# Optimization experiments

Measured on AMD Instinct MI355X. Metric: run time of the kernel, lower is better.

The kernel has to match this reference:

```python
import jax, jax.numpy as jnp
import numpy as np

B, C, N, M, H = 2, 512, 2048, 2048, 8
HD = C // H
SCALE = HD ** -0.5


def setup_inputs() -> dict:
    key = jax.random.key(0)
    ks = jax.random.split(key, 8)
    x = jax.random.normal(ks[0], (B, C, N), dtype=jnp.float32)
    y = jax.random.normal(ks[1], (B, C, M), dtype=jnp.float32)
    # linear weights stored as [in, out] so out = in @ W (equivalent to torch Linear)
    Wq = jax.random.normal(ks[2], (C, C), dtype=jnp.float32) * (C ** -0.5)
    Wkv = jax.random.normal(ks[3], (C, 2 * C), dtype=jnp.float32) * (C ** -0.5)
    # depthwise Conv1d, kernel_size=1, groups=C -> per-channel scale + bias
    lw = jax.random.normal(ks[4], (C,), dtype=jnp.float32)
    lb = jax.random.normal(ks[5], (C,), dtype=jnp.float32) * 0.01
    Wp = jax.random.normal(ks[6], (C, C), dtype=jnp.float32) * (C ** -0.5)
    bp = jax.random.normal(ks[7], (C,), dtype=jnp.float32) * 0.01
    return {"x": x, "y": y, "Wq": Wq, "Wkv": Wkv, "lw": lw, "lb": lb, "Wp": Wp, "bp": bp}


def reference(x, y, Wq, Wkv, lw, lb, Wp, bp):
    # x: [B,C,N], y: [B,C,M]
    q = (x.transpose(0, 2, 1) @ Wq).reshape(B, N, H, HD).transpose(0, 2, 1, 3)  # [B,H,N,HD]
    kv = (y.transpose(0, 2, 1) @ Wkv).reshape(B, M, H, HD, 2).transpose(0, 2, 1, 3, 4)
    k, v = kv[..., 0], kv[..., 1]  # [B,H,M,HD]
    attn = jax.nn.softmax(jnp.einsum('bhnd,bhmd->bhnm', q, k) * SCALE, axis=-1)
    # depthwise conv1d (ksize=1) on v laid out as [B,C,M]; channel c = h*HD + d
    lw2 = lw.reshape(H, HD)[None, :, None, :]
    lb2 = lb.reshape(H, HD)[None, :, None, :]
    v = v + v * lw2 + lb2
    out = jnp.einsum('bhnm,bhmd->bhnd', attn, v).transpose(0, 2, 1, 3).reshape(B, N, C)
    out = (out @ Wp + bp).transpose(0, 2, 1)  # [B,C,N]
    return out
```

## Files before the change

### kernel.cpp

```cpp
#include <hip/hip_runtime.h>

#define Bb 2
#define Cc 512
#define Nn 2048
#define Mm 2048
#define Hh 8
#define HD 64
#define QSCALE 0.18033688011112042f

typedef unsigned short u16;
typedef unsigned int u32;
typedef __bf16 bf16x8 __attribute__((ext_vector_type(8)));
typedef float f32x16 __attribute__((ext_vector_type(16)));

union V4 {
    uint4 u;
    bf16x8 b;
};

__device__ __forceinline__ u16 f2bfu(float f) {
    unsigned int b = __float_as_uint(f);
    unsigned int r = (b + 0x7fffu + ((b >> 16) & 1u)) >> 16;
    return (u16)r;
}
__device__ __forceinline__ float bfu2f(u16 u) {
    return __uint_as_float(((unsigned int)u) << 16);
}
__device__ __forceinline__ u32 pkbf(float lo, float hi_) {
    return __builtin_amdgcn_perm(__float_as_uint(hi_) + 0x8000u,
                                 __float_as_uint(lo) + 0x8000u, 0x07060302u);
}

__global__ __launch_bounds__(256) void transpose_xy(const float* __restrict__ x,
                                                    const float* __restrict__ y,
                                                    u16* __restrict__ xT,
                                                    u16* __restrict__ yT) {
    __shared__ float tile[32][33];
    const int z = blockIdx.z;
    const float* in = (z < 2) ? x : y;
    u16* out = (z < 2) ? xT : yT;
    const int b = z & 1;
    const int R = 512, S = 2048;
    size_t base = (size_t)b * R * S;
    int r0 = blockIdx.y * 32, s0 = blockIdx.x * 32;
    int tx = threadIdx.x, ty = threadIdx.y;
#pragma unroll
    for (int k = 0; k < 4; k++)
        tile[ty + 8 * k][tx] = in[base + (size_t)(r0 + ty + 8 * k) * S + s0 + tx];
    __syncthreads();
#pragma unroll
    for (int k = 0; k < 4; k++)
        out[base + (size_t)(s0 + ty + 8 * k) * R + r0 + tx] = f2bfu(tile[tx][ty + 8 * k]);
}

__global__ __launch_bounds__(256) void transpose_w(const float* __restrict__ Wq,
                                                   const float* __restrict__ Wkv,
                                                   const float* __restrict__ Wp,
                                                   u16* __restrict__ WqT,
                                                   u16* __restrict__ WkvT,
                                                   u16* __restrict__ WpT) {
    __shared__ float tile[32][33];
    const int bx = blockIdx.x;
    const float* in;
    u16* out;
    int S, sx;
    if (bx < 16) {
        in = Wq; out = WqT; S = 512; sx = bx;
    } else if (bx < 48) {
        in = Wkv; out = WkvT; S = 1024; sx = bx - 16;
    } else {
        in = Wp; out = WpT; S = 512; sx = bx - 48;
    }
    const int R = 512;
    int r0 = blockIdx.y * 32, s0 = sx * 32;
    int tx = threadIdx.x, ty = threadIdx.y;
#pragma unroll
    for (int k = 0; k < 4; k++)
        tile[ty + 8 * k][tx] = in[(size_t)(r0 + ty + 8 * k) * S + s0 + tx];
    __syncthreads();
#pragma unroll
    for (int k = 0; k < 4; k++)
        out[(size_t)(s0 + ty + 8 * k) * R + r0 + tx] = f2bfu(tile[tx][ty + 8 * k]);
}

template <int MODE>
__global__ __launch_bounds__(256) void gemm_nt(const u16* __restrict__ A,
                                               const u16* __restrict__ Bt,
                                               u16* __restrict__ outp, int Ncols) {
    __shared__ alignas(16) u16 As[2][128 * 64];
    __shared__ alignas(16) u16 Bs[2][64 * 64];
    const int t = threadIdx.x;
    const int lane = t & 63, w = t >> 6;
    const int r = lane & 31, hi = lane >> 5;
    const int r0 = blockIdx.y * 128, c0 = blockIdx.x * 64;
    const int wr = (w & 1) * 64, wc = (w >> 1) * 32;

    const int sra = t >> 3, ska = t & 7;
    const int swa = ((ska ^ (sra & 7)) << 3);
    const u16* Ag = A + (size_t)(r0 + sra) * 512 + ska * 8;
    const u16* Bg = Bt + (size_t)(c0 + sra) * 512 + ska * 8;

    {
#pragma unroll
        for (int i = 0; i < 4; i++)
            *(uint4*)&As[0][(sra + 32 * i) * 64 + swa] = *(const uint4*)(Ag + (size_t)i * 32 * 512);
#pragma unroll
        for (int i = 0; i < 2; i++)
            *(uint4*)&Bs[0][(sra + 32 * i) * 64 + swa] = *(const uint4*)(Bg + (size_t)i * 32 * 512);
    }
    __syncthreads();

    f32x16 acc[2];
#pragma unroll
    for (int rs = 0; rs < 2; rs++)
#pragma unroll
        for (int e = 0; e < 16; e++) acc[rs][e] = 0.f;

    const int ra0 = wr + r, ra1 = wr + 32 + r, rb = wc + r;

    for (int kk = 0; kk < 8; kk++) {
        const int cur = kk & 1;
        uint4 pa[4], pb[2];
        const bool more = (kk < 7);
        if (more) {
            const size_t ko = (size_t)(kk + 1) * 64;
#pragma unroll
            for (int i = 0; i < 4; i++) pa[i] = *(const uint4*)(Ag + (size_t)i * 32 * 512 + ko);
#pragma unroll
            for (int i = 0; i < 2; i++) pb[i] = *(const uint4*)(Bg + (size_t)i * 32 * 512 + ko);
        }
        V4 af[2][4], bf[4];
#pragma unroll
        for (int ks = 0; ks < 4; ks++) {
            const int c = 2 * ks + hi;
            bf[ks].u = *(const uint4*)&Bs[cur][rb * 64 + ((c ^ (rb & 7)) << 3)];
            af[0][ks].u = *(const uint4*)&As[cur][ra0 * 64 + ((c ^ (ra0 & 7)) << 3)];
            af[1][ks].u = *(const uint4*)&As[cur][ra1 * 64 + ((c ^ (ra1 & 7)) << 3)];
        }
#pragma unroll
        for (int ks = 0; ks < 4; ks++) {
            acc[0] = __builtin_amdgcn_mfma_f32_32x32x16_bf16(af[0][ks].b, bf[ks].b, acc[0], 0, 0, 0);
            acc[1] = __builtin_amdgcn_mfma_f32_32x32x16_bf16(af[1][ks].b, bf[ks].b, acc[1], 0, 0, 0);
        }
        if (more) {
            const int nxt = cur ^ 1;
#pragma unroll
            for (int i = 0; i < 4; i++) *(uint4*)&As[nxt][(sra + 32 * i) * 64 + swa] = pa[i];
#pragma unroll
            for (int i = 0; i < 2; i++) *(uint4*)&Bs[nxt][(sra + 32 * i) * 64 + swa] = pb[i];
        }
        __syncthreads();
    }

    const int cg = c0 + wc + r;
#pragma unroll
    for (int rs = 0; rs < 2; rs++)
#pragma unroll
        for (int e = 0; e < 16; e++) {
            int m = r0 + wr + rs * 32 + 4 * hi + (e & 3) + 8 * (e >> 2);
            float v = acc[rs][e];
            if constexpr (MODE == 3) v *= QSCALE;
            outp[(size_t)m * Ncols + cg] = f2bfu(v);
        }
}

__global__ __launch_bounds__(256) void gemm_out(const u16* __restrict__ Wt,
                                                const u16* __restrict__ Ob,
                                                float* __restrict__ out,
                                                const float* __restrict__ bias) {
    __shared__ alignas(16) u16 Ws[2][64 * 64];
    __shared__ alignas(16) u16 Os[2][128 * 64];
    const int t = threadIdx.x;
    const int lane = t & 63, w = t >> 6;
    const int r = lane & 31, hi = lane >> 5;
    const int c0 = blockIdx.x * 64, n0 = blockIdx.y * 128;
    const int cb = (w & 1) * 32, nb = (w >> 1) * 32;

    const int sra = t >> 3, ska = t & 7;
    const int swa = ((ska ^ (sra & 7)) << 3);
    const u16* Wg = Wt + (size_t)(c0 + sra) * 512 + ska * 8;
    const u16* Og = Ob + (size_t)(n0 + sra) * 512 + ska * 8;

    {
#pragma unroll
        for (int i = 0; i < 2; i++)
            *(uint4*)&Ws[0][(sra + 32 * i) * 64 + swa] = *(const uint4*)(Wg + (size_t)i * 32 * 512);
#pragma unroll
        for (int i = 0; i < 4; i++)
            *(uint4*)&Os[0][(sra + 32 * i) * 64 + swa] = *(const uint4*)(Og + (size_t)i * 32 * 512);
    }
    __syncthreads();

    f32x16 acc[2];
#pragma unroll
    for (int ns = 0; ns < 2; ns++)
#pragma unroll
        for (int e = 0; e < 16; e++) acc[ns][e] = 0.f;

    const int rw = cb + r, ro0 = nb + r, ro1 = nb + 64 + r;

    for (int kk = 0; kk < 8; kk++) {
        const int cur = kk & 1;
        uint4 pw[2], po_[4];
        const bool more = (kk < 7);
        if (more) {
            const size_t ko = (size_t)(kk + 1) * 64;
#pragma unroll
            for (int i = 0; i < 2; i++) pw[i] = *(const uint4*)(Wg + (size_t)i * 32 * 512 + ko);
#pragma unroll
            for (int i = 0; i < 4; i++) po_[i] = *(const uint4*)(Og + (size_t)i * 32 * 512 + ko);
        }
        V4 wf[4], of[2][4];
#pragma unroll
        for (int ks = 0; ks < 4; ks++) {
            const int c = 2 * ks + hi;
            wf[ks].u = *(const uint4*)&Ws[cur][rw * 64 + ((c ^ (rw & 7)) << 3)];
            of[0][ks].u = *(const uint4*)&Os[cur][ro0 * 64 + ((c ^ (ro0 & 7)) << 3)];
            of[1][ks].u = *(const uint4*)&Os[cur][ro1 * 64 + ((c ^ (ro1 & 7)) << 3)];
        }
#pragma unroll
        for (int ks = 0; ks < 4; ks++) {
            acc[0] = __builtin_amdgcn_mfma_f32_32x32x16_bf16(wf[ks].b, of[0][ks].b, acc[0], 0, 0, 0);
            acc[1] = __builtin_amdgcn_mfma_f32_32x32x16_bf16(wf[ks].b, of[1][ks].b, acc[1], 0, 0, 0);
        }
        if (more) {
            const int nxt = cur ^ 1;
#pragma unroll
            for (int i = 0; i < 2; i++) *(uint4*)&Ws[nxt][(sra + 32 * i) * 64 + swa] = pw[i];
#pragma unroll
            for (int i = 0; i < 4; i++) *(uint4*)&Os[nxt][(sra + 32 * i) * 64 + swa] = po_[i];
        }
        __syncthreads();
    }

#pragma unroll
    for (int e = 0; e < 16; e++) {
        const int c_r = c0 + cb + 4 * hi + (e & 3) + 8 * (e >> 2);
        const float bv = bias[c_r];
#pragma unroll
        for (int ns = 0; ns < 2; ns++) {
            const int rg = n0 + nb + ns * 64 + r;
            const int b = rg >> 11, n = rg & 2047;
            out[((size_t)b * 512 + c_r) * 2048 + n] = acc[ns][e] + bv;
        }
    }
}

__global__ __launch_bounds__(256) void split_kv(const u16* __restrict__ kv,
                                                const float* __restrict__ lw,
                                                const float* __restrict__ lb,
                                                u16* __restrict__ kout,
                                                u16* __restrict__ vtout) {
    __shared__ u16 vtile[64][72];
    int t = threadIdx.x;
    int m0 = blockIdx.x * 64, h = blockIdx.y, b = blockIdx.z;
    int mr = t >> 2, d0 = (t & 3) * 16;
    const u16* row = kv + ((size_t)(b * Mm + m0 + mr)) * 1024 + (h * 64 + d0) * 2;
    size_t kob = ((size_t)((b * Hh + h) * Mm) + m0 + mr) * 64 + d0;
#pragma unroll
    for (int i = 0; i < 16; i++) {
        int c = h * 64 + d0 + i;
        u16 kb = row[2 * i];
        float vv = bfu2f(row[2 * i + 1]);
        float vp = vv + vv * lw[c] + lb[c];
        kout[kob + i] = kb;
        vtile[d0 + i][mr] = f2bfu(vp);
    }
    __syncthreads();
    int dd = t >> 2, mg = (t & 3) * 16;
    size_t vob = ((size_t)((b * Hh + h) * 64) + dd) * Mm + m0 + mg;
#pragma unroll
    for (int i = 0; i < 16; i++) vtout[vob + i] = vtile[dd][mg + i];
}

__global__ __launch_bounds__(256, 4) void flash_attn(const u16* __restrict__ q,
                                                     const u16* __restrict__ kk,
                                                     const u16* __restrict__ vt,
                                                     float* __restrict__ po,
                                                     float* __restrict__ ls) {
    __shared__ alignas(16) u16 Ks[2][64 * 64];
    __shared__ alignas(16) u16 Vs[2][64 * 64];
    const int t = threadIdx.x;
    const int lane = t & 63, w = t >> 6;
    const int r = lane & 31, hi = lane >> 5;
    const int nt = blockIdx.x & 15, sp = blockIdx.x >> 4;
    const int h = blockIdx.y, b = blockIdx.z;
    const int bh = b * Hh + h;
    const int nw = nt * 128 + 32 * w + r;
    const int MT0 = sp * 8, MT1 = MT0 + 8;

    V4 qf[4];
    {
        const u16* qrow = q + ((size_t)(b * Nn + nw)) * Cc + h * HD + hi * 8;
#pragma unroll
        for (int ks = 0; ks < 4; ks++) qf[ks].u = *(const uint4*)(qrow + ks * 16);
    }

    const u16* kbase = kk + ((size_t)bh) * Mm * HD;
    const u16* vbase = vt + ((size_t)bh) * HD * Mm;

    const int cr0 = t >> 3, cc0 = t & 7;
    const int cr1 = cr0 + 32, cc1 = cc0;
    const int swa0 = cr0 * 64 + ((cc0 ^ (cr0 & 7)) << 3);
    const int swa1 = cr1 * 64 + ((cc1 ^ (cr1 & 7)) << 3);

    {
        int m00 = MT0 * 64;
        uint4 a0 = *(const uint4*)(kbase + (size_t)(m00 + cr0) * HD + cc0 * 8);
        uint4 a1 = *(const uint4*)(kbase + (size_t)(m00 + cr1) * HD + cc1 * 8);
        uint4 b0 = *(const uint4*)(vbase + (size_t)cr0 * Mm + m00 + cc0 * 8);
        uint4 b1 = *(const uint4*)(vbase + (size_t)cr1 * Mm + m00 + cc1 * 8);
        *(uint4*)&Ks[0][swa0] = a0;
        *(uint4*)&Ks[0][swa1] = a1;
        *(uint4*)&Vs[0][swa0] = b0;
        *(uint4*)&Vs[0][swa1] = b1;
    }
    __syncthreads();

    f32x16 oa0, oa1;
#pragma unroll
    for (int e = 0; e < 16; e++) {
        oa0[e] = 0.f;
        oa1[e] = 0.f;
    }
    float lsum = 0.f;

    for (int mt = MT0; mt < MT1; mt++) {
        const int cur = mt & 1;
        uint4 nk0, nk1, nv0, nv1;
        const bool more = (mt + 1 < MT1);
        if (more) {
            int m0 = (mt + 1) * 64;
            nk0 = *(const uint4*)(kbase + (size_t)(m0 + cr0) * HD + cc0 * 8);
            nk1 = *(const uint4*)(kbase + (size_t)(m0 + cr1) * HD + cc1 * 8);
            nv0 = *(const uint4*)(vbase + (size_t)cr0 * Mm + m0 + cc0 * 8);
            nv1 = *(const uint4*)(vbase + (size_t)cr1 * Mm + m0 + cc1 * 8);
        }
        f32x16 sa[2];
#pragma unroll
        for (int s = 0; s < 2; s++) {
#pragma unroll
            for (int e = 0; e < 16; e++) sa[s][e] = 0.f;
#pragma unroll
            for (int ks = 0; ks < 4; ks++) {
                V4 af;
                af.u = *(const uint4*)&Ks[cur][(32 * s + r) * 64 +
                                               (((2 * ks + hi) ^ (r & 7)) << 3)];
                sa[s] = __builtin_amdgcn_mfma_f32_32x32x16_bf16(af.b, qf[ks].b, sa[s], 0, 0, 0);
            }
        }
#pragma unroll
        for (int s = 0; s < 2; s++) {
            u32 p[8];
#pragma unroll
            for (int qq = 0; qq < 8; qq++) {
                float e0 = __builtin_amdgcn_exp2f(sa[s][2 * qq]);
                float e1 = __builtin_amdgcn_exp2f(sa[s][2 * qq + 1]);
                lsum += e0 + e1;
                p[qq] = pkbf(e0, e1);
            }
            u32 xr0 = __shfl_xor(hi ? p[0] : p[2], 32);
            u32 xr1 = __shfl_xor(hi ? p[1] : p[3], 32);
            u32 xr2 = __shfl_xor(hi ? p[4] : p[6], 32);
            u32 xr3 = __shfl_xor(hi ? p[5] : p[7], 32);
#pragma unroll
            for (int kl = 0; kl < 2; kl++) {
                V4 pf;
                if (kl == 0) {
                    pf.u.x = hi ? xr0 : p[0];
                    pf.u.y = hi ? xr1 : p[1];
                    pf.u.z = hi ? p[2] : xr0;
                    pf.u.w = hi ? p[3] : xr1;
                } else {
                    pf.u.x = hi ? xr2 : p[4];
                    pf.u.y = hi ? xr3 : p[5];
                    pf.u.z = hi ? p[6] : xr2;
                    pf.u.w = hi ? p[7] : xr3;
                }
                const int c = 4 * s + 2 * kl + hi;
                V4 vf0, vf1;
                vf0.u = *(const uint4*)&Vs[cur][r * 64 + ((c ^ (r & 7)) << 3)];
                vf1.u = *(const uint4*)&Vs[cur][(32 + r) * 64 + ((c ^ (r & 7)) << 3)];
                oa0 = __builtin_amdgcn_mfma_f32_32x32x16_bf16(vf0.b, pf.b, oa0, 0, 0, 0);
                oa1 = __builtin_amdgcn_mfma_f32_32x32x16_bf16(vf1.b, pf.b, oa1, 0, 0, 0);
            }
        }
        if (more) {
            const int nxt = cur ^ 1;
            *(uint4*)&Ks[nxt][swa0] = nk0;
            *(uint4*)&Ks[nxt][swa1] = nk1;
            *(uint4*)&Vs[nxt][swa0] = nv0;
            *(uint4*)&Vs[nxt][swa1] = nv1;
        }
        __syncthreads();
    }

    lsum += __shfl_xor(lsum, 32);
    float* pob = po + (((size_t)sp * 16 + bh) * 64) * 2048 + nw;
#pragma unroll
    for (int e = 0; e < 16; e++) {
        int d0 = (e & 3) + 8 * (e >> 2) + 4 * hi;
        pob[(size_t)d0 * 2048] = oa0[e];
        pob[(size_t)(d0 + 32) * 2048] = oa1[e];
    }
    if (hi == 0) ls[((size_t)sp * 16 + bh) * 2048 + nw] = lsum;
}

__global__ __launch_bounds__(256) void combine_o(const float* __restrict__ po,
                                                 const float* __restrict__ ls,
                                                 u16* __restrict__ o) {
    __shared__ u16 tile[64][72];
    const int t = threadIdx.x;
    const int n0 = blockIdx.x * 64, bh = blockIdx.y;
    const int n = n0 + (t & 63), dg = t >> 6;
    float linv;
    {
        float s = 0.f;
#pragma unroll
        for (int sp = 0; sp < 4; sp++) s += ls[((size_t)sp * 16 + bh) * 2048 + n];
        linv = 1.0f / s;
    }
#pragma unroll
    for (int i = 0; i < 16; i++) {
        int d = dg * 16 + i;
        float acc = 0.f;
#pragma unroll
        for (int sp = 0; sp < 4; sp++)
            acc += po[(((size_t)sp * 16 + bh) * 64 + d) * 2048 + n];
        tile[t & 63][d] = f2bfu(acc * linv);
    }
    __syncthreads();
    const int nr = t >> 2, dq = (t & 3) * 16;
    const int b = bh >> 3, h = bh & 7;
    u16* orow = o + ((size_t)(b * Nn + n0 + nr)) * Cc + h * 64 + dq;
    *(uint4*)(orow + 0) = *(const uint4*)&tile[nr][dq];
    *(uint4*)(orow + 8) = *(const uint4*)&tile[nr][dq + 8];
}

static const size_t OFF_XT = 0;
static const size_t OFF_YT = 4194304;
static const size_t OFF_WQT = 8388608;
static const size_t OFF_WKVT = 8912896;
static const size_t OFF_WPT = 9961472;
static const size_t OFF_Q = 10485760;
static const size_t OFF_KV = 14680064;
static const size_t OFF_K = 23068672;
static const size_t OFF_VT = 27262976;
static const size_t OFF_O = 31457280;
static const size_t OFF_PO = 35651584;
static const size_t OFF_LS = 69206016;

extern "C" void kernel_launch(void* const* d_in, const int* in_sizes, int n_in,
                              void* d_out, int out_size, void* d_ws, size_t ws_size,
                              hipStream_t stream) {
    const float* x = (const float*)d_in[0];
    const float* y = (const float*)d_in[1];
    const float* Wq = (const float*)d_in[2];
    const float* Wkv = (const float*)d_in[3];
    const float* lw = (const float*)d_in[4];
    const float* lb = (const float*)d_in[5];
    const float* Wp = (const float*)d_in[6];
    const float* bp = (const float*)d_in[7];

    char* ws = (char*)d_ws;
    u16* xT = (u16*)(ws + OFF_XT);
    u16* yT = (u16*)(ws + OFF_YT);
    u16* WqT = (u16*)(ws + OFF_WQT);
    u16* WkvT = (u16*)(ws + OFF_WKVT);
    u16* WpT = (u16*)(ws + OFF_WPT);
    u16* qb = (u16*)(ws + OFF_Q);
    u16* kvb = (u16*)(ws + OFF_KV);
    u16* kb = (u16*)(ws + OFF_K);
    u16* vtb = (u16*)(ws + OFF_VT);
    u16* ob = (u16*)(ws + OFF_O);
    float* po = (float*)(ws + OFF_PO);
    float* lsw = (float*)(ws + OFF_LS);

    dim3 tb(32, 8, 1);
    transpose_xy<<<dim3(64, 16, 4), tb, 0, stream>>>(x, y, xT, yT);
    transpose_w<<<dim3(64, 16), tb, 0, stream>>>(Wq, Wkv, Wp, WqT, WkvT, WpT);

    gemm_nt<3><<<dim3(8, 32), 256, 0, stream>>>(xT, WqT, qb, 512);
    gemm_nt<0><<<dim3(16, 32), 256, 0, stream>>>(yT, WkvT, kvb, 1024);

    split_kv<<<dim3(Mm / 64, Hh, Bb), 256, 0, stream>>>(kvb, lw, lb, kb, vtb);

    flash_attn<<<dim3(64, Hh, Bb), 256, 0, stream>>>(qb, kb, vtb, po, lsw);
    combine_o<<<dim3(Nn / 64, Bb * Hh), 256, 0, stream>>>(po, lsw, ob);

    gemm_out<<<dim3(8, 32), 256, 0, stream>>>(WpT, ob, (float*)d_out, bp);
}
```

Measured before the change: 157.6 us.

## Merge transposes, fuse Q/KV projections with K/V split and depthwise scale

Combines the activation and weight transpose kernels into one launch, and merges the Q and KV projection GEMMs into a single launch. The KV epilogue now writes K in per-head layout and V transposed with the depthwise scale and bias applied directly, which removes the split_kv kernel and the intermediate kv buffer round trip. This cuts three launches and one full read/write pass over the KV tensor. The cost is strided scattered epilogue stores for K and V and some branch divergence between Q and KV blocks.

```diff
diff --git a/kernel.cpp b/kernel.cpp
--- a/kernel.cpp
+++ b/kernel.cpp
@@ -23,26 +23,38 @@
     unsigned int r = (b + 0x7fffu + ((b >> 16) & 1u)) >> 16;
     return (u16)r;
 }
-__device__ __forceinline__ float bfu2f(u16 u) {
-    return __uint_as_float(((unsigned int)u) << 16);
-}
 __device__ __forceinline__ u32 pkbf(float lo, float hi_) {
     return __builtin_amdgcn_perm(__float_as_uint(hi_) + 0x8000u,
                                  __float_as_uint(lo) + 0x8000u, 0x07060302u);
 }
 
-__global__ __launch_bounds__(256) void transpose_xy(const float* __restrict__ x,
-                                                    const float* __restrict__ y,
-                                                    u16* __restrict__ xT,
-                                                    u16* __restrict__ yT) {
+__global__ __launch_bounds__(256) void transpose_all(
+    const float* __restrict__ x, const float* __restrict__ y, const float* __restrict__ Wq,
+    const float* __restrict__ Wkv, const float* __restrict__ Wp, u16* __restrict__ xT,
+    u16* __restrict__ yT, u16* __restrict__ WqT, u16* __restrict__ WkvT,
+    u16* __restrict__ WpT) {
     __shared__ float tile[32][33];
     const int z = blockIdx.z;
-    const float* in = (z < 2) ? x : y;
-    u16* out = (z < 2) ? xT : yT;
-    const int b = z & 1;
-    const int R = 512, S = 2048;
-    size_t base = (size_t)b * R * S;
-    int r0 = blockIdx.y * 32, s0 = blockIdx.x * 32;
+    const float* in;
+    u16* out;
+    int S, sx = blockIdx.x;
+    size_t base = 0;
+    const int R = 512;
+    if (z < 4) {
+        in = (z < 2) ? x : y;
+        out = (z < 2) ? xT : yT;
+        S = 2048;
+        base = (size_t)(z & 1) * R * S;
+    } else {
+        if (sx < 16) {
+            in = Wq; out = WqT; S = 512;
+        } else if (sx < 48) {
+            in = Wkv; out = WkvT; S = 1024; sx -= 16;
+        } else {
+            in = Wp; out = WpT; S = 512; sx -= 48;
+        }
+    }
+    int r0 = blockIdx.y * 32, s0 = sx * 32;
     int tx = threadIdx.x, ty = threadIdx.y;
 #pragma unroll
     for (int k = 0; k < 4; k++)
@@ -53,47 +65,25 @@
         out[base + (size_t)(s0 + ty + 8 * k) * R + r0 + tx] = f2bfu(tile[tx][ty + 8 * k]);
 }
 
-__global__ __launch_bounds__(256) void transpose_w(const float* __restrict__ Wq,
-                                                   const float* __restrict__ Wkv,
-                                                   const float* __restrict__ Wp,
-                                                   u16* __restrict__ WqT,
-                                                   u16* __restrict__ WkvT,
-                                                   u16* __restrict__ WpT) {
-    __shared__ float tile[32][33];
-    const int bx = blockIdx.x;
-    const float* in;
-    u16* out;
-    int S, sx;
-    if (bx < 16) {
-        in = Wq; out = WqT; S = 512; sx = bx;
-    } else if (bx < 48) {
-        in = Wkv; out = WkvT; S = 1024; sx = bx - 16;
-    } else {
-        in = Wp; out = WpT; S = 512; sx = bx - 48;
-    }
-    const int R = 512;
-    int r0 = blockIdx.y * 32, s0 = sx * 32;
-    int tx = threadIdx.x, ty = threadIdx.y;
-#pragma unroll
-    for (int k = 0; k < 4; k++)
-        tile[ty + 8 * k][tx] = in[(size_t)(r0 + ty + 8 * k) * S + s0 + tx];
-    __syncthreads();
-#pragma unroll
-    for (int k = 0; k < 4; k++)
-        out[(size_t)(s0 + ty + 8 * k) * R + r0 + tx] = f2bfu(tile[tx][ty + 8 * k]);
-}
-
-template <int MODE>
-__global__ __launch_bounds__(256) void gemm_nt(const u16* __restrict__ A,
-                                               const u16* __restrict__ Bt,
-                                               u16* __restrict__ outp, int Ncols) {
+__global__ __launch_bounds__(256) void proj_qkv(const u16* __restrict__ xT,
+                                                const u16* __restrict__ yT,
+                                                const u16* __restrict__ WqT,
+                                                const u16* __restrict__ WkvT,
+                                                const float* __restrict__ lw,
+                                                const float* __restrict__ lb,
+                                                u16* __restrict__ qb, u16* __restrict__ kb,
+                                                u16* __restrict__ vtb) {
     __shared__ alignas(16) u16 As[2][128 * 64];
     __shared__ alignas(16) u16 Bs[2][64 * 64];
     const int t = threadIdx.x;
     const int lane = t & 63, w = t >> 6;
     const int r = lane & 31, hi = lane >> 5;
-    const int r0 = blockIdx.y * 128, c0 = blockIdx.x * 64;
+    const bool isQ = (blockIdx.x < 8);
+    const int c0 = (isQ ? blockIdx.x : blockIdx.x - 8) * 64;
+    const int r0 = blockIdx.y * 128;
     const int wr = (w & 1) * 64, wc = (w >> 1) * 32;
+    const u16* A = isQ ? xT : yT;
+    const u16* Bt = isQ ? WqT : WkvT;
 
     const int sra = t >> 3, ska = t & 7;
     const int swa = ((ska ^ (sra & 7)) << 3);
@@ -153,124 +143,47 @@
     }
 
     const int cg = c0 + wc + r;
-#pragma unroll
-    for (int rs = 0; rs < 2; rs++)
-#pragma unroll
-        for (int e = 0; e < 16; e++) {
-            int m = r0 + wr + rs * 32 + 4 * hi + (e & 3) + 8 * (e >> 2);
-            float v = acc[rs][e];
-            if constexpr (MODE == 3) v *= QSCALE;
-            outp[(size_t)m * Ncols + cg] = f2bfu(v);
-        }
-}
-
-__global__ __launch_bounds__(256) void gemm_out(const u16* __restrict__ Wt,
-                                                const u16* __restrict__ Ob,
-                                                float* __restrict__ out,
-                                                const float* __restrict__ bias) {
-    __shared__ alignas(16) u16 Ws[2][64 * 64];
-    __shared__ alignas(16) u16 Os[2][128 * 64];
-    const int t = threadIdx.x;
-    const int lane = t & 63, w = t >> 6;
-    const int r = lane & 31, hi = lane >> 5;
-    const int c0 = blockIdx.x * 64, n0 = blockIdx.y * 128;
-    const int cb = (w & 1) * 32, nb = (w >> 1) * 32;
-
-    const int sra = t >> 3, ska = t & 7;
-    const int swa = ((ska ^ (sra & 7)) << 3);
-    const u16* Wg = Wt + (size_t)(c0 + sra) * 512 + ska * 8;
-    const u16* Og = Ob + (size_t)(n0 + sra) * 512 + ska * 8;
-
-    {
-#pragma unroll
-        for (int i = 0; i < 2; i++)
-            *(uint4*)&Ws[0][(sra + 32 * i) * 64 + swa] = *(const uint4*)(Wg + (size_t)i * 32 * 512);
-#pragma unroll
-        for (int i = 0; i < 4; i++)
-            *(uint4*)&Os[0][(sra + 32 * i) * 64 + swa] = *(const uint4*)(Og + (size_t)i * 32 * 512);
-    }
-    __syncthreads();
-
-    f32x16 acc[2];
-#pragma unroll
-    for (int ns = 0; ns < 2; ns++)
-#pragma unroll
-        for (int e = 0; e < 16; e++) acc[ns][e] = 0.f;
-
-    const int rw = cb + r, ro0 = nb + r, ro1 = nb + 64 + r;
-
-    for (int kk = 0; kk < 8; kk++) {
-        const int cur = kk & 1;
-        uint4 pw[2], po_[4];
-        const bool more = (kk < 7);
-        if (more) {
-            const size_t ko = (size_t)(kk + 1) * 64;
-#pragma unroll
-            for (int i = 0; i < 2; i++) pw[i] = *(const uint4*)(Wg + (size_t)i * 32 * 512 + ko);
-#pragma unroll
-            for (int i = 0; i < 4; i++) po_[i] = *(const uint4*)(Og + (size_t)i * 32 * 512 + ko);
-        }
-        V4 wf[4], of[2][4];
-#pragma unroll
-        for (int ks = 0; ks < 4; ks++) {
-            const int c = 2 * ks + hi;
-            wf[ks].u = *(const uint4*)&Ws[cur][rw * 64 + ((c ^ (rw & 7)) << 3)];
-            of[0][ks].u = *(const uint4*)&Os[cur][ro0 * 64 + ((c ^ (ro0 & 7)) << 3)];
-            of[1][ks].u = *(const uint4*)&Os[cur][ro1 * 64 + ((c ^ (ro1 & 7)) << 3)];
-        }
-#pragma unroll
-        for (int ks = 0; ks < 4; ks++) {
-            acc[0] = __builtin_amdgcn_mfma_f32_32x32x16_bf16(wf[ks].b, of[0][ks].b, acc[0], 0, 0, 0);
-            acc[1] = __builtin_amdgcn_mfma_f32_32x32x16_bf16(wf[ks].b, of[1][ks].b, acc[1], 0, 0, 0);
-        }
-        if (more) {
-            const int nxt = cur ^ 1;
-#pragma unroll
-            for (int i = 0; i < 2; i++) *(uint4*)&Ws[nxt][(sra + 32 * i) * 64 + swa] = pw[i];
-#pragma unroll
-            for (int i = 0; i < 4; i++) *(uint4*)&Os[nxt][(sra + 32 * i) * 64 + swa] = po_[i];
-        }
-        __syncthreads();
-    }
-
-#pragma unroll
-    for (int e = 0; e < 16; e++) {
-        const int c_r = c0 + cb + 4 * hi + (e & 3) + 8 * (e >> 2);
-        const float bv = bias[c_r];
-#pragma unroll
-        for (int ns = 0; ns < 2; ns++) {
-            const int rg = n0 + nb + ns * 64 + r;
-            const int b = rg >> 11, n = rg & 2047;
-            out[((size_t)b * 512 + c_r) * 2048 + n] = acc[ns][e] + bv;
-        }
-    }
-}
-
-__global__ __launch_bounds__(256) void split_kv(const u16* __restrict__ kv,
-                                                const float* __restrict__ lw,
-                                                const float* __restrict__ lb,
-                                                u16* __restrict__ kout,
-                                                u16* __restrict__ vtout) {
-    __shared__ u16 vtile[64][72];
-    int t = threadIdx.x;
-    int m0 = blockIdx.x * 64, h = blockIdx.y, b = blockIdx.z;
-    int mr = t >> 2, d0 = (t & 3) * 16;
-    const u16* row = kv + ((size_t)(b * Mm + m0 + mr)) * 1024 + (h * 64 + d0) * 2;
-    size_t kob = ((size_t)((b * Hh + h) * Mm) + m0 + mr) * 64 + d0;
-#pragma unroll
-    for (int i = 0; i < 16; i++) {
-        int c = h * 64 + d0 + i;
-        u16 kb = row[2 * i];
-        float vv = bfu2f(row[2 * i + 1]);
-        float vp = vv + vv * lw[c] + lb[c];
-        kout[kob + i] = kb;
-        vtile[d0 + i][mr] = f2bfu(vp);
-    }
-    __syncthreads();
-    int dd = t >> 2, mg = (t & 3) * 16;
-    size_t vob = ((size_t)((b * Hh + h) * 64) + dd) * Mm + m0 + mg;
-#pragma unroll
-    for (int i = 0; i < 16; i++) vtout[vob + i] = vtile[dd][mg + i];
+    if (isQ) {
+#pragma unroll
+        for (int rs = 0; rs < 2; rs++)
+#pragma unroll
+            for (int e = 0; e < 16; e++) {
+                int m = r0 + wr + rs * 32 + 4 * hi + (e & 3) + 8 * (e >> 2);
+                qb[(size_t)m * 512 + cg] = f2bfu(acc[rs][e] * QSCALE);
+            }
+    } else {
+        const int hd = cg >> 1, s = cg & 1, h = hd >> 6, d = hd & 63;
+        const int bq = r0 >> 11;
+        const int bh = bq * 8 + h;
+        const int mb = (r0 & 2047) + wr + 4 * hi;
+        if (s == 0) {
+            u16* kbase = kb + ((size_t)bh * 2048) * 64 + d;
+#pragma unroll
+            for (int rs = 0; rs < 2; rs++)
+#pragma unroll
+                for (int e = 0; e < 16; e++) {
+                    int m = mb + rs * 32 + (e & 3) + 8 * (e >> 2);
+                    kbase[(size_t)m * 64] = f2bfu(acc[rs][e]);
+                }
+        } else {
+            const float sw = 1.0f + lw[hd], sb = lb[hd];
+            u16* vbase = vtb + ((size_t)bh * 64 + d) * 2048;
+#pragma unroll
+            for (int rs = 0; rs < 2; rs++)
+#pragma unroll
+                for (int eg = 0; eg < 4; eg++) {
+                    int m = mb + rs * 32 + 8 * eg;
+                    float v0 = acc[rs][4 * eg + 0] * sw + sb;
+                    float v1 = acc[rs][4 * eg + 1] * sw + sb;
+                    float v2 = acc[rs][4 * eg + 2] * sw + sb;
+                    float v3 = acc[rs][4 * eg + 3] * sw + sb;
+                    uint2 pk;
+                    pk.x = pkbf(v0, v1);
+                    pk.y = pkbf(v2, v3);
+                    *(uint2*)(vbase + m) = pk;
+                }
+        }
+    }
 }
 
 __global__ __launch_bounds__(256, 4) void flash_attn(const u16* __restrict__ q,
@@ -437,13 +350,94 @@
     *(uint4*)(orow + 8) = *(const uint4*)&tile[nr][dq + 8];
 }
 
+__global__ __launch_bounds__(256) void gemm_out(const u16* __restrict__ Wt,
+                                                const u16* __restrict__ Ob,
+                                                float* __restrict__ out,
+                                                const float* __restrict__ bias) {
+    __shared__ alignas(16) u16 Ws[2][64 * 64];
+    __shared__ alignas(16) u16 Os[2][128 * 64];
+    const int t = threadIdx.x;
+    const int lane = t & 63, w = t >> 6;
+    const int r = lane & 31, hi = lane >> 5;
+    const int c0 = blockIdx.x * 64, n0 = blockIdx.y * 128;
+    const int cb = (w & 1) * 32, nb = (w >> 1) * 32;
+
+    const int sra = t >> 3, ska = t & 7;
+    const int swa = ((ska ^ (sra & 7)) << 3);
+    const u16* Wg = Wt + (size_t)(c0 + sra) * 512 + ska * 8;
+    const u16* Og = Ob + (size_t)(n0 + sra) * 512 + ska * 8;
+
+    {
+#pragma unroll
+        for (int i = 0; i < 2; i++)
+            *(uint4*)&Ws[0][(sra + 32 * i) * 64 + swa] = *(const uint4*)(Wg + (size_t)i * 32 * 512);
+#pragma unroll
+        for (int i = 0; i < 4; i++)
+            *(uint4*)&Os[0][(sra + 32 * i) * 64 + swa] = *(const uint4*)(Og + (size_t)i * 32 * 512);
+    }
+    __syncthreads();
+
+    f32x16 acc[2];
+#pragma unroll
+    for (int ns = 0; ns < 2; ns++)
+#pragma unroll
+        for (int e = 0; e < 16; e++) acc[ns][e] = 0.f;
+
+    const int rw = cb + r, ro0 = nb + r, ro1 = nb + 64 + r;
+
+    for (int kk = 0; kk < 8; kk++) {
+        const int cur = kk & 1;
+        uint4 pw[2], po_[4];
+        const bool more = (kk < 7);
+        if (more) {
+            const size_t ko = (size_t)(kk + 1) * 64;
+#pragma unroll
+            for (int i = 0; i < 2; i++) pw[i] = *(const uint4*)(Wg + (size_t)i * 32 * 512 + ko);
+#pragma unroll
+            for (int i = 0; i < 4; i++) po_[i] = *(const uint4*)(Og + (size_t)i * 32 * 512 + ko);
+        }
+        V4 wf[4], of[2][4];
+#pragma unroll
+        for (int ks = 0; ks < 4; ks++) {
+            const int c = 2 * ks + hi;
+            wf[ks].u = *(const uint4*)&Ws[cur][rw * 64 + ((c ^ (rw & 7)) << 3)];
+            of[0][ks].u = *(const uint4*)&Os[cur][ro0 * 64 + ((c ^ (ro0 & 7)) << 3)];
+            of[1][ks].u = *(const uint4*)&Os[cur][ro1 * 64 + ((c ^ (ro1 & 7)) << 3)];
+        }
+#pragma unroll
+        for (int ks = 0; ks < 4; ks++) {
+            acc[0] = __builtin_amdgcn_mfma_f32_32x32x16_bf16(wf[ks].b, of[0][ks].b, acc[0], 0, 0, 0);
+            acc[1] = __builtin_amdgcn_mfma_f32_32x32x16_bf16(wf[ks].b, of[1][ks].b, acc[1], 0, 0, 0);
+        }
+        if (more) {
+            const int nxt = cur ^ 1;
+#pragma unroll
+            for (int i = 0; i < 2; i++) *(uint4*)&Ws[nxt][(sra + 32 * i) * 64 + swa] = pw[i];
+#pragma unroll
+            for (int i = 0; i < 4; i++) *(uint4*)&Os[nxt][(sra + 32 * i) * 64 + swa] = po_[i];
+        }
+        __syncthreads();
+    }
+
+#pragma unroll
+    for (int e = 0; e < 16; e++) {
+        const int c_r = c0 + cb + 4 * hi + (e & 3) + 8 * (e >> 2);
+        const float bv = bias[c_r];
+#pragma unroll
+        for (int ns = 0; ns < 2; ns++) {
+            const int rg = n0 + nb + ns * 64 + r;
+            const int b = rg >> 11, n = rg & 2047;
+            out[((size_t)b * 512 + c_r) * 2048 + n] = acc[ns][e] + bv;
+        }
+    }
+}
+
 static const size_t OFF_XT = 0;
 static const size_t OFF_YT = 4194304;
 static const size_t OFF_WQT = 8388608;
 static const size_t OFF_WKVT = 8912896;
 static const size_t OFF_WPT = 9961472;
 static const size_t OFF_Q = 10485760;
-static const size_t OFF_KV = 14680064;
 static const size_t OFF_K = 23068672;
 static const size_t OFF_VT = 27262976;
 static const size_t OFF_O = 31457280;
@@ -469,7 +463,6 @@
     u16* WkvT = (u16*)(ws + OFF_WKVT);
     u16* WpT = (u16*)(ws + OFF_WPT);
     u16* qb = (u16*)(ws + OFF_Q);
-    u16* kvb = (u16*)(ws + OFF_KV);
     u16* kb = (u16*)(ws + OFF_K);
     u16* vtb = (u16*)(ws + OFF_VT);
     u16* ob = (u16*)(ws + OFF_O);
@@ -477,16 +470,10 @@
     float* lsw = (float*)(ws + OFF_LS);
 
     dim3 tb(32, 8, 1);
-    transpose_xy<<<dim3(64, 16, 4), tb, 0, stream>>>(x, y, xT, yT);
-    transpose_w<<<dim3(64, 16), tb, 0, stream>>>(Wq, Wkv, Wp, WqT, WkvT, WpT);
-
-    gemm_nt<3><<<dim3(8, 32), 256, 0, stream>>>(xT, WqT, qb, 512);
-    gemm_nt<0><<<dim3(16, 32), 256, 0, stream>>>(yT, WkvT, kvb, 1024);
-
-    split_kv<<<dim3(Mm / 64, Hh, Bb), 256, 0, stream>>>(kvb, lw, lb, kb, vtb);
-
+    transpose_all<<<dim3(64, 16, 5), tb, 0, stream>>>(x, y, Wq, Wkv, Wp, xT, yT, WqT, WkvT,
+                                                      WpT);
+    proj_qkv<<<dim3(24, 32), 256, 0, stream>>>(xT, yT, WqT, WkvT, lw, lb, qb, kb, vtb);
     flash_attn<<<dim3(64, Hh, Bb), 256, 0, stream>>>(qb, kb, vtb, po, lsw);
     combine_o<<<dim3(Nn / 64, Bb * Hh), 256, 0, stream>>>(po, lsw, ob);
-
     gemm_out<<<dim3(8, 32), 256, 0, stream>>>(WpT, ob, (float*)d_out, bp);
 }
```

After: 142.6 us. 1.11x faster.
